# Optimization experiments

Hardware: AMD Instinct MI355X
Metric: run time of the kernel (lower is better)

## Reference

```python
import jax, jax.numpy as jnp
from jax import lax
import numpy as np

INPUT = 80
H1 = 100
H2 = 50


def _lstm_layer(x, Wih, Whh, bih, bhh):
    """PyTorch-semantics single-layer LSTM, batch_first.
    x: [B,T,I]; Wih: [4H,I]; Whh: [4H,H]; biases: [4H]. Gate order: i,f,g,o.
    Returns full hidden sequence [B,T,H]."""
    B, T, _ = x.shape
    H = Whh.shape[1]
    # precompute input projections for all timesteps (one big GEMM)
    pre = jnp.einsum('bti,gi->tbg', x, Wih) + (bih + bhh)  # [T,B,4H]

    def step(carry, p):
        h, c = carry
        gates = p + h @ Whh.T  # [B,4H]
        i, f, g, o = jnp.split(gates, 4, axis=-1)
        i = jax.nn.sigmoid(i)
        f = jax.nn.sigmoid(f)
        g = jnp.tanh(g)
        o = jax.nn.sigmoid(o)
        c = f * c + i * g
        h = o * jnp.tanh(c)
        return (h, c), h

    h0 = jnp.zeros((B, H), x.dtype)
    (_, _), hs = lax.scan(step, (h0, h0), pre)  # hs: [T,B,H]
    return jnp.transpose(hs, (1, 0, 2))  # [B,T,H]


def setup_inputs() -> dict:
    key = jax.random.key(0)
    ks = jax.random.split(key, 9)
    B, T = 1024, 512
    s1 = 1.0 / np.sqrt(H1)
    s2 = 1.0 / np.sqrt(H2)
    return {
        'x': jax.random.normal(ks[0], (B, T, INPUT), dtype=jnp.float32),
        'Wih1': jax.random.uniform(ks[1], (4 * H1, INPUT), jnp.float32, -s1, s1),
        'Whh1': jax.random.uniform(ks[2], (4 * H1, H1), jnp.float32, -s1, s1),
        'bih1': jax.random.uniform(ks[3], (4 * H1,), jnp.float32, -s1, s1),
        'bhh1': jax.random.uniform(ks[4], (4 * H1,), jnp.float32, -s1, s1),
        'Wih2': jax.random.uniform(ks[5], (4 * H2, H1), jnp.float32, -s2, s2),
        'Whh2': jax.random.uniform(ks[6], (4 * H2, H2), jnp.float32, -s2, s2),
        'bih2': jax.random.uniform(ks[7], (4 * H2,), jnp.float32, -s2, s2),
        'bhh2': jax.random.uniform(ks[8], (4 * H2,), jnp.float32, -s2, s2),
    }


def reference(x, Wih1, Whh1, bih1, bhh1, Wih2, Whh2, bih2, bhh2):
    # Dropout layers are identity in eval mode.
    h1 = _lstm_layer(x, Wih1, Whh1, bih1, bhh1)   # [B,T,100]
    h2 = _lstm_layer(h1, Wih2, Whh2, bih2, bhh2)  # [B,T,50]
    return h2[:, -1, :]                            # [B,50]
```

## Files before the change

kernel.cpp:

```cpp
#include <hip/hip_runtime.h>

#define BT 1024
#define TT 512

__device__ __forceinline__ float sig_(float x) { return 1.f / (1.f + __expf(-x)); }
__device__ __forceinline__ float th_(float x)  { return 1.f - 2.f / (1.f + __expf(2.f * x)); }

template <int KS, int KPAD, int KH, int N, bool XMODE>
__device__ __forceinline__ void gp_stage(
    const float* __restrict__ A, const float* __restrict__ W,
    float (&As)[128][KPAD], float (&Bs)[KPAD][128],
    int tid, int n0, int by, int t0, int k0)
{
    constexpr int NQH = KH / 4;
#pragma unroll
    for (int ii = tid; ii < 128 * NQH; ii += 256) {
        int r = ii / NQH, q = ii % NQH;
        const float* src;
        if (XMODE) {
            int b  = (by & 7) * 128 + r;
            int tl = by >> 3;
            src = A + ((size_t)b * TT + (t0 + tl)) * KS;
        } else {
            src = A + (size_t)(by * 128 + r) * KS;
        }
        *(float4*)&As[r][q * 4] = *(const float4*)(src + k0 + q * 4);
    }
#pragma unroll
    for (int ii = tid; ii < 128 * NQH; ii += 256) {
        int n = ii & 127, kq = ii >> 7;
        float4 v = make_float4(0.f, 0.f, 0.f, 0.f);
        if (n0 + n < N) v = *(const float4*)(W + (size_t)(n0 + n) * KS + k0 + kq * 4);
        Bs[kq * 4 + 0][n] = v.x; Bs[kq * 4 + 1][n] = v.y;
        Bs[kq * 4 + 2][n] = v.z; Bs[kq * 4 + 3][n] = v.w;
    }
}

template <int KPAD, int KH>
__device__ __forceinline__ void gp_compute(
    const float (&As)[128][KPAD], const float (&Bs)[KPAD][128],
    float (&acc)[8][8], int tx, int ty)
{
    for (int kk = 0; kk < KH; kk += 4) {
        float4 bv[4][2];
#pragma unroll
        for (int r = 0; r < 4; r++) {
            bv[r][0] = *(const float4*)&Bs[kk + r][tx * 8];
            bv[r][1] = *(const float4*)&Bs[kk + r][tx * 8 + 4];
        }
#pragma unroll
        for (int i = 0; i < 8; i++) {
            float4 av = *(const float4*)&As[ty + 16 * i][kk];
#pragma unroll
            for (int s = 0; s < 2; s++) {
                acc[i][s*4+0] = fmaf(av.x, bv[0][s].x, acc[i][s*4+0]);
                acc[i][s*4+0] = fmaf(av.y, bv[1][s].x, acc[i][s*4+0]);
                acc[i][s*4+0] = fmaf(av.z, bv[2][s].x, acc[i][s*4+0]);
                acc[i][s*4+0] = fmaf(av.w, bv[3][s].x, acc[i][s*4+0]);
                acc[i][s*4+1] = fmaf(av.x, bv[0][s].y, acc[i][s*4+1]);
                acc[i][s*4+1] = fmaf(av.y, bv[1][s].y, acc[i][s*4+1]);
                acc[i][s*4+1] = fmaf(av.z, bv[2][s].y, acc[i][s*4+1]);
                acc[i][s*4+1] = fmaf(av.w, bv[3][s].y, acc[i][s*4+1]);
                acc[i][s*4+2] = fmaf(av.x, bv[0][s].z, acc[i][s*4+2]);
                acc[i][s*4+2] = fmaf(av.y, bv[1][s].z, acc[i][s*4+2]);
                acc[i][s*4+2] = fmaf(av.z, bv[2][s].z, acc[i][s*4+2]);
                acc[i][s*4+2] = fmaf(av.w, bv[3][s].z, acc[i][s*4+2]);
                acc[i][s*4+3] = fmaf(av.x, bv[0][s].w, acc[i][s*4+3]);
                acc[i][s*4+3] = fmaf(av.y, bv[1][s].w, acc[i][s*4+3]);
                acc[i][s*4+3] = fmaf(av.z, bv[2][s].w, acc[i][s*4+3]);
                acc[i][s*4+3] = fmaf(av.w, bv[3][s].w, acc[i][s*4+3]);
            }
        }
    }
}

template <int KS, int KPAD, int KH0, int N, bool XMODE>
__global__ __launch_bounds__(256, 3) void gemm_pre(
    const float* __restrict__ A, const float* __restrict__ W,
    const float* __restrict__ bih, const float* __restrict__ bhh,
    float* __restrict__ out, int t0)
{
    constexpr int KH1 = KS - KH0;
    __shared__ __align__(16) float As[128][KPAD];
    __shared__ __align__(16) float Bs[KPAD][128];
    const int tid = threadIdx.x;
    const int n0 = blockIdx.x * 128;
    const int by = blockIdx.y;
    const int Rbase = by * 128;
    const int tx = tid & 15, ty = tid >> 4;

    float acc[8][8];
#pragma unroll
    for (int i = 0; i < 8; i++)
#pragma unroll
        for (int j = 0; j < 8; j++) acc[i][j] = 0.f;

    gp_stage<KS, KPAD, KH0, N, XMODE>(A, W, As, Bs, tid, n0, by, t0, 0);
    __syncthreads();
    gp_compute<KPAD, KH0>(As, Bs, acc, tx, ty);
    __syncthreads();
    gp_stage<KS, KPAD, KH1, N, XMODE>(A, W, As, Bs, tid, n0, by, t0, KH0);
    __syncthreads();
    gp_compute<KPAD, KH1>(As, Bs, acc, tx, ty);

#pragma unroll
    for (int s = 0; s < 2; s++) {
        int n = n0 + tx * 8 + s * 4;
        if (n < N) {
            float4 bias;
            bias.x = bih[n] + bhh[n];         bias.y = bih[n + 1] + bhh[n + 1];
            bias.z = bih[n + 2] + bhh[n + 2]; bias.w = bih[n + 3] + bhh[n + 3];
#pragma unroll
            for (int i = 0; i < 8; i++) {
                size_t R = (size_t)Rbase + ty + 16 * i;
                float4 o;
                o.x = acc[i][s*4+0] + bias.x; o.y = acc[i][s*4+1] + bias.y;
                o.z = acc[i][s*4+2] + bias.z; o.w = acc[i][s*4+3] + bias.w;
                *(float4*)(out + R * N + n) = o;
            }
        }
    }
}

__global__ __launch_bounds__(512, 4) void rec1(
    const float* __restrict__ pre,
    const float* __restrict__ Whh,
    float* __restrict__ hseq,
    float* __restrict__ cst,
    int Tc, int first)
{
    __shared__ __align__(16) float hs[2][100];
    __shared__ __align__(16) float pres[2][800];
    __shared__ float gbuf[5 * 4 * 2 * 100];
    const int tid = threadIdx.x;
    const int b0 = blockIdx.x * 2;

    const bool comp = tid < 500;
    const int j  = tid % 100;
    const int kq = tid / 100;

    float4 w[4][5];
    if (comp) {
#pragma unroll
        for (int g = 0; g < 4; g++) {
            const float4* W4 = (const float4*)(Whh + (size_t)(g * 100 + j) * 100);
#pragma unroll
            for (int q = 0; q < 5; q++) w[g][q] = W4[kq * 5 + q];
        }
    }

    const bool upd = tid < 200;
    const int ub = tid / 100, uj = tid % 100;
    float c = 0.f;
    if (upd) {
        float h = 0.f;
        if (!first) {
            h = hseq[((size_t)(Tc - 1) * BT + b0 + ub) * 100 + uj];
            c = cst[(size_t)(b0 + ub) * 100 + uj];
        }
        hs[ub][uj] = h;
        ((float4*)pres[0])[tid] = ((const float4*)(pre + (size_t)b0 * 400))[tid];
    }
    __syncthreads();

    int cur = 0;
    for (int t = 0; t < Tc; t++) {
        int tn = (t + 1 < Tc) ? (t + 1) : t;
        float4 pf0;
        if (upd)
            pf0 = ((const float4*)(pre + (size_t)tn * BT * 400 + (size_t)b0 * 400))[tid];

        if (comp) {
            float acc[4][2];
#pragma unroll
            for (int g = 0; g < 4; g++) { acc[g][0] = 0.f; acc[g][1] = 0.f; }
            const float4* h0 = (const float4*)hs[0];
            const float4* h1 = (const float4*)hs[1];
#pragma unroll
            for (int q = 0; q < 5; q++) {
                int f = kq * 5 + q;
                float4 v0 = h0[f], v1 = h1[f];
#pragma unroll
                for (int g = 0; g < 4; g++) {
                    float4 wq = w[g][q];
                    acc[g][0] = fmaf(wq.x, v0.x, acc[g][0]);
                    acc[g][0] = fmaf(wq.y, v0.y, acc[g][0]);
                    acc[g][0] = fmaf(wq.z, v0.z, acc[g][0]);
                    acc[g][0] = fmaf(wq.w, v0.w, acc[g][0]);
                    acc[g][1] = fmaf(wq.x, v1.x, acc[g][1]);
                    acc[g][1] = fmaf(wq.y, v1.y, acc[g][1]);
                    acc[g][1] = fmaf(wq.z, v1.z, acc[g][1]);
                    acc[g][1] = fmaf(wq.w, v1.w, acc[g][1]);
                }
            }
#pragma unroll
            for (int g = 0; g < 4; g++) {
                gbuf[((kq * 4 + g) * 2 + 0) * 100 + j] = acc[g][0];
                gbuf[((kq * 4 + g) * 2 + 1) * 100 + j] = acc[g][1];
            }
        }
        __syncthreads();

        if (upd) {
            const float* pb = pres[cur];
            float s0 = 0.f, s1 = 0.f, s2 = 0.f, s3 = 0.f;
#pragma unroll
            for (int q = 0; q < 5; q++) {
                int base = q * 800;
                s0 += gbuf[base + (0 * 2 + ub) * 100 + uj];
                s1 += gbuf[base + (1 * 2 + ub) * 100 + uj];
                s2 += gbuf[base + (2 * 2 + ub) * 100 + uj];
                s3 += gbuf[base + (3 * 2 + ub) * 100 + uj];
            }
            float xi = s0 + pb[ub * 400 + uj];
            float xf = s1 + pb[ub * 400 + 100 + uj];
            float xg = s2 + pb[ub * 400 + 200 + uj];
            float xo = s3 + pb[ub * 400 + 300 + uj];
            float ii = sig_(xi), ff = sig_(xf), gg = th_(xg), oo = sig_(xo);
            c = ff * c + ii * gg;
            float h = oo * th_(c);
            hs[ub][uj] = h;
            hseq[((size_t)t * BT + b0 + ub) * 100 + uj] = h;
            ((float4*)pres[cur ^ 1])[tid] = pf0;
        }
        __syncthreads();
        cur ^= 1;
    }
    if (upd) cst[(size_t)(b0 + ub) * 100 + uj] = c;
}

__global__ __launch_bounds__(256, 4) void rec2(
    const float* __restrict__ pre2,
    const float* __restrict__ Whh,
    float* __restrict__ cst, float* __restrict__ hst,
    float* __restrict__ out,
    int Tc, int first)
{
    __shared__ __align__(16) float hs[2][50];
    __shared__ __align__(16) float pres[2][400];
    __shared__ float gbuf[5 * 4 * 2 * 50];
    const int tid = threadIdx.x;
    const int b0 = blockIdx.x * 2;

    const bool comp = tid < 250;
    const int j  = tid % 50;
    const int kq = tid / 50;

    float2 w[4][5];
    if (comp) {
#pragma unroll
        for (int g = 0; g < 4; g++) {
            const float2* W2 = (const float2*)(Whh + (size_t)(g * 50 + j) * 50);
#pragma unroll
            for (int q = 0; q < 5; q++) w[g][q] = W2[kq * 5 + q];
        }
    }

    const bool upd = tid < 100;
    const int ub = tid / 50, uj = tid % 50;
    float c = 0.f, hlast = 0.f;
    if (upd) {
        float h = 0.f;
        if (!first) {
            h = hst[(size_t)(b0 + ub) * 50 + uj];
            c = cst[(size_t)(b0 + ub) * 50 + uj];
        }
        hs[ub][uj] = h;
        hlast = h;
        ((float4*)pres[0])[tid] = ((const float4*)(pre2 + (size_t)b0 * 200))[tid];
    }
    __syncthreads();

    int cur = 0;
    for (int t = 0; t < Tc; t++) {
        int tn = (t + 1 < Tc) ? (t + 1) : t;
        float4 pf0;
        if (upd)
            pf0 = ((const float4*)(pre2 + (size_t)tn * BT * 200 + (size_t)b0 * 200))[tid];

        if (comp) {
            float acc[4][2];
#pragma unroll
            for (int g = 0; g < 4; g++) { acc[g][0] = 0.f; acc[g][1] = 0.f; }
            const float2* hA = (const float2*)hs[0];
            const float2* hB = (const float2*)hs[1];
#pragma unroll
            for (int q = 0; q < 5; q++) {
                int f = kq * 5 + q;
                float2 v0 = hA[f], v1 = hB[f];
#pragma unroll
                for (int g = 0; g < 4; g++) {
                    float2 wq = w[g][q];
                    acc[g][0] = fmaf(wq.x, v0.x, acc[g][0]);
                    acc[g][0] = fmaf(wq.y, v0.y, acc[g][0]);
                    acc[g][1] = fmaf(wq.x, v1.x, acc[g][1]);
                    acc[g][1] = fmaf(wq.y, v1.y, acc[g][1]);
                }
            }
#pragma unroll
            for (int g = 0; g < 4; g++) {
                gbuf[((kq * 4 + g) * 2 + 0) * 50 + j] = acc[g][0];
                gbuf[((kq * 4 + g) * 2 + 1) * 50 + j] = acc[g][1];
            }
        }
        __syncthreads();

        if (upd) {
            const float* pb = pres[cur];
            float s0 = 0.f, s1 = 0.f, s2 = 0.f, s3 = 0.f;
#pragma unroll
            for (int q = 0; q < 5; q++) {
                int base = q * 400;
                s0 += gbuf[base + (0 * 2 + ub) * 50 + uj];
                s1 += gbuf[base + (1 * 2 + ub) * 50 + uj];
                s2 += gbuf[base + (2 * 2 + ub) * 50 + uj];
                s3 += gbuf[base + (3 * 2 + ub) * 50 + uj];
            }
            float xi = s0 + pb[ub * 200 + uj];
            float xf = s1 + pb[ub * 200 + 50 + uj];
            float xg = s2 + pb[ub * 200 + 100 + uj];
            float xo = s3 + pb[ub * 200 + 150 + uj];
            float ii = sig_(xi), ff = sig_(xf), gg = th_(xg), oo = sig_(xo);
            c = ff * c + ii * gg;
            float h = oo * th_(c);
            hs[ub][uj] = h;
            hlast = h;
            ((float4*)pres[cur ^ 1])[tid] = pf0;
        }
        __syncthreads();
        cur ^= 1;
    }
    if (upd) {
        cst[(size_t)(b0 + ub) * 50 + uj] = c;
        hst[(size_t)(b0 + ub) * 50 + uj] = hlast;
        out[(size_t)(b0 + ub) * 50 + uj] = hlast;
    }
}

extern "C" void kernel_launch(void* const* d_in, const int* in_sizes, int n_in,
                              void* d_out, int out_size, void* d_ws, size_t ws_size,
                              hipStream_t stream)
{
    const float* x    = (const float*)d_in[0];
    const float* Wih1 = (const float*)d_in[1];
    const float* Whh1 = (const float*)d_in[2];
    const float* bih1 = (const float*)d_in[3];
    const float* bhh1 = (const float*)d_in[4];
    const float* Wih2 = (const float*)d_in[5];
    const float* Whh2 = (const float*)d_in[6];
    const float* bih2 = (const float*)d_in[7];
    const float* bhh2 = (const float*)d_in[8];
    float* out = (float*)d_out;
    float* ws  = (float*)d_ws;

    int Tc = 64;
    auto need = [](int tc) -> size_t {
        return ((size_t)tc * 1024 * (400 + 100 + 200) +
                (size_t)1024 * 100 + (size_t)1024 * 50 * 2) * sizeof(float);
    };
    while (Tc > 1 && need(Tc) > ws_size) Tc >>= 1;

    float* pre1 = ws;
    float* h1s  = pre1 + (size_t)Tc * 1024 * 400;
    float* pre2 = h1s  + (size_t)Tc * 1024 * 100;
    float* c1   = pre2 + (size_t)Tc * 1024 * 200;
    float* c2   = c1 + 1024 * 100;
    float* h2st = c2 + 1024 * 50;

    const int nch = TT / Tc;
    for (int ch = 0; ch < nch; ch++) {
        int t0 = ch * Tc;
        gemm_pre<80, 40, 40, 400, true ><<<dim3(4, Tc * 8), 256, 0, stream>>>(
            x, Wih1, bih1, bhh1, pre1, t0);
        rec1<<<dim3(512), dim3(512), 0, stream>>>(pre1, Whh1, h1s, c1, Tc, ch == 0 ? 1 : 0);
        gemm_pre<100, 52, 52, 200, false><<<dim3(2, Tc * 8), 256, 0, stream>>>(
            h1s, Wih2, bih2, bhh2, pre2, 0);
        rec2<<<dim3(512), dim3(256), 0, stream>>>(pre2, Whh2, c2, h2st, out, Tc, ch == 0 ? 1 : 0);
    }
}
```

Baseline: 2.529 ms.

## Overlap layer-2 recurrence of previous chunk with layer-1 recurrence in fused kernel

Moves the two LSTM recurrence bodies into device functions that share one shared-memory union. A combined kernel runs layer-1 on chunk ch in its first 512 blocks and layer-2 on chunk ch-1 in 256 extra blocks, each handling two 256-thread groups. The launch order becomes a software pipeline: prologue, steady state, epilogue, with the layer-2 input GEMM issued before pre1 is overwritten. The goal is to hide the latency-bound sequential recurrences of both layers behind each other instead of running them back to back. The cost is more complex chunk dependencies and a larger grid competing for CU resources.

```diff
diff --git a/kernel.cpp b/kernel.cpp
--- a/kernel.cpp
+++ b/kernel.cpp
@@ -122,19 +122,23 @@
     }
 }
 
-__global__ __launch_bounds__(512, 4) void rec1(
-    const float* __restrict__ pre,
-    const float* __restrict__ Whh,
-    float* __restrict__ hseq,
-    float* __restrict__ cst,
-    int Tc, int first)
-{
-    __shared__ __align__(16) float hs[2][100];
-    __shared__ __align__(16) float pres[2][800];
-    __shared__ float gbuf[5 * 4 * 2 * 100];
-    const int tid = threadIdx.x;
-    const int b0 = blockIdx.x * 2;
-
+struct __align__(16) R1S {
+    float hs[2][100];
+    float pres[2][800];
+    float gbuf[5 * 4 * 2 * 100];
+};
+struct __align__(16) R2S {
+    float hs[2][50];
+    float pres[2][400];
+    float gbuf[5 * 4 * 2 * 50];
+};
+union __align__(16) FS { R1S r1; R2S r2[2]; };
+
+__device__ __forceinline__ void rec1_body(
+    R1S& s, int tid, int b0,
+    const float* __restrict__ pre, const float* __restrict__ Whh,
+    float* __restrict__ hseq, float* __restrict__ cst, int Tc, int first)
+{
     const bool comp = tid < 500;
     const int j  = tid % 100;
     const int kq = tid / 100;
@@ -158,8 +162,8 @@
             h = hseq[((size_t)(Tc - 1) * BT + b0 + ub) * 100 + uj];
             c = cst[(size_t)(b0 + ub) * 100 + uj];
         }
-        hs[ub][uj] = h;
-        ((float4*)pres[0])[tid] = ((const float4*)(pre + (size_t)b0 * 400))[tid];
+        s.hs[ub][uj] = h;
+        ((float4*)s.pres[0])[tid] = ((const float4*)(pre + (size_t)b0 * 400))[tid];
     }
     __syncthreads();
 
@@ -174,8 +178,8 @@
             float acc[4][2];
 #pragma unroll
             for (int g = 0; g < 4; g++) { acc[g][0] = 0.f; acc[g][1] = 0.f; }
-            const float4* h0 = (const float4*)hs[0];
-            const float4* h1 = (const float4*)hs[1];
+            const float4* h0 = (const float4*)s.hs[0];
+            const float4* h1 = (const float4*)s.hs[1];
 #pragma unroll
             for (int q = 0; q < 5; q++) {
                 int f = kq * 5 + q;
@@ -195,22 +199,22 @@
             }
 #pragma unroll
             for (int g = 0; g < 4; g++) {
-                gbuf[((kq * 4 + g) * 2 + 0) * 100 + j] = acc[g][0];
-                gbuf[((kq * 4 + g) * 2 + 1) * 100 + j] = acc[g][1];
+                s.gbuf[((kq * 4 + g) * 2 + 0) * 100 + j] = acc[g][0];
+                s.gbuf[((kq * 4 + g) * 2 + 1) * 100 + j] = acc[g][1];
             }
         }
         __syncthreads();
 
         if (upd) {
-            const float* pb = pres[cur];
+            const float* pb = s.pres[cur];
             float s0 = 0.f, s1 = 0.f, s2 = 0.f, s3 = 0.f;
 #pragma unroll
             for (int q = 0; q < 5; q++) {
                 int base = q * 800;
-                s0 += gbuf[base + (0 * 2 + ub) * 100 + uj];
-                s1 += gbuf[base + (1 * 2 + ub) * 100 + uj];
-                s2 += gbuf[base + (2 * 2 + ub) * 100 + uj];
-                s3 += gbuf[base + (3 * 2 + ub) * 100 + uj];
+                s0 += s.gbuf[base + (0 * 2 + ub) * 100 + uj];
+                s1 += s.gbuf[base + (1 * 2 + ub) * 100 + uj];
+                s2 += s.gbuf[base + (2 * 2 + ub) * 100 + uj];
+                s3 += s.gbuf[base + (3 * 2 + ub) * 100 + uj];
             }
             float xi = s0 + pb[ub * 400 + uj];
             float xf = s1 + pb[ub * 400 + 100 + uj];
@@ -219,9 +223,9 @@
             float ii = sig_(xi), ff = sig_(xf), gg = th_(xg), oo = sig_(xo);
             c = ff * c + ii * gg;
             float h = oo * th_(c);
-            hs[ub][uj] = h;
+            s.hs[ub][uj] = h;
             hseq[((size_t)t * BT + b0 + ub) * 100 + uj] = h;
-            ((float4*)pres[cur ^ 1])[tid] = pf0;
+            ((float4*)s.pres[cur ^ 1])[tid] = pf0;
         }
         __syncthreads();
         cur ^= 1;
@@ -229,19 +233,12 @@
     if (upd) cst[(size_t)(b0 + ub) * 100 + uj] = c;
 }
 
-__global__ __launch_bounds__(256, 4) void rec2(
-    const float* __restrict__ pre2,
-    const float* __restrict__ Whh,
-    float* __restrict__ cst, float* __restrict__ hst,
-    float* __restrict__ out,
+__device__ __forceinline__ void rec2_body(
+    R2S& s, int tid, int b0,
+    const float* __restrict__ pre2, const float* __restrict__ Whh,
+    float* __restrict__ cst, float* __restrict__ hst, float* __restrict__ out,
     int Tc, int first)
 {
-    __shared__ __align__(16) float hs[2][50];
-    __shared__ __align__(16) float pres[2][400];
-    __shared__ float gbuf[5 * 4 * 2 * 50];
-    const int tid = threadIdx.x;
-    const int b0 = blockIdx.x * 2;
-
     const bool comp = tid < 250;
     const int j  = tid % 50;
     const int kq = tid / 50;
@@ -265,9 +262,9 @@
             h = hst[(size_t)(b0 + ub) * 50 + uj];
             c = cst[(size_t)(b0 + ub) * 50 + uj];
         }
-        hs[ub][uj] = h;
+        s.hs[ub][uj] = h;
         hlast = h;
-        ((float4*)pres[0])[tid] = ((const float4*)(pre2 + (size_t)b0 * 200))[tid];
+        ((float4*)s.pres[0])[tid] = ((const float4*)(pre2 + (size_t)b0 * 200))[tid];
     }
     __syncthreads();
 
@@ -282,8 +279,8 @@
             float acc[4][2];
 #pragma unroll
             for (int g = 0; g < 4; g++) { acc[g][0] = 0.f; acc[g][1] = 0.f; }
-            const float2* hA = (const float2*)hs[0];
-            const float2* hB = (const float2*)hs[1];
+            const float2* hA = (const float2*)s.hs[0];
+            const float2* hB = (const float2*)s.hs[1];
 #pragma unroll
             for (int q = 0; q < 5; q++) {
                 int f = kq * 5 + q;
@@ -299,22 +296,22 @@
             }
 #pragma unroll
             for (int g = 0; g < 4; g++) {
-                gbuf[((kq * 4 + g) * 2 + 0) * 50 + j] = acc[g][0];
-                gbuf[((kq * 4 + g) * 2 + 1) * 50 + j] = acc[g][1];
+                s.gbuf[((kq * 4 + g) * 2 + 0) * 50 + j] = acc[g][0];
+                s.gbuf[((kq * 4 + g) * 2 + 1) * 50 + j] = acc[g][1];
             }
         }
         __syncthreads();
 
         if (upd) {
-            const float* pb = pres[cur];
+            const float* pb = s.pres[cur];
             float s0 = 0.f, s1 = 0.f, s2 = 0.f, s3 = 0.f;
 #pragma unroll
             for (int q = 0; q < 5; q++) {
                 int base = q * 400;
-                s0 += gbuf[base + (0 * 2 + ub) * 50 + uj];
-                s1 += gbuf[base + (1 * 2 + ub) * 50 + uj];
-                s2 += gbuf[base + (2 * 2 + ub) * 50 + uj];
-                s3 += gbuf[base + (3 * 2 + ub) * 50 + uj];
+                s0 += s.gbuf[base + (0 * 2 + ub) * 50 + uj];
+                s1 += s.gbuf[base + (1 * 2 + ub) * 50 + uj];
+                s2 += s.gbuf[base + (2 * 2 + ub) * 50 + uj];
+                s3 += s.gbuf[base + (3 * 2 + ub) * 50 + uj];
             }
             float xi = s0 + pb[ub * 200 + uj];
             float xf = s1 + pb[ub * 200 + 50 + uj];
@@ -323,9 +320,9 @@
             float ii = sig_(xi), ff = sig_(xf), gg = th_(xg), oo = sig_(xo);
             c = ff * c + ii * gg;
             float h = oo * th_(c);
-            hs[ub][uj] = h;
+            s.hs[ub][uj] = h;
             hlast = h;
-            ((float4*)pres[cur ^ 1])[tid] = pf0;
+            ((float4*)s.pres[cur ^ 1])[tid] = pf0;
         }
         __syncthreads();
         cur ^= 1;
@@ -335,6 +332,34 @@
         hst[(size_t)(b0 + ub) * 50 + uj] = hlast;
         out[(size_t)(b0 + ub) * 50 + uj] = hlast;
     }
+}
+
+__global__ __launch_bounds__(512, 4) void rec_fused(
+    const float* __restrict__ pre1, const float* __restrict__ Whh1,
+    float* __restrict__ h1seq, float* __restrict__ c1, int first1,
+    const float* __restrict__ pre2, const float* __restrict__ Whh2,
+    float* __restrict__ c2, float* __restrict__ h2st, float* __restrict__ out,
+    int first2, int Tc)
+{
+    __shared__ FS sm;
+    const int bx = blockIdx.x;
+    const int tid = threadIdx.x;
+    if (bx < 512) {
+        rec1_body(sm.r1, tid, bx * 2, pre1, Whh1, h1seq, c1, Tc, first1);
+    } else {
+        const int h = tid >> 8;
+        rec2_body(sm.r2[h], tid & 255, (bx - 512) * 4 + h * 2,
+                  pre2, Whh2, c2, h2st, out, Tc, first2);
+    }
+}
+
+__global__ __launch_bounds__(256, 4) void rec2k(
+    const float* __restrict__ pre2, const float* __restrict__ Whh,
+    float* __restrict__ cst, float* __restrict__ hst, float* __restrict__ out,
+    int Tc, int first)
+{
+    __shared__ R2S s;
+    rec2_body(s, threadIdx.x, blockIdx.x * 2, pre2, Whh, cst, hst, out, Tc, first);
 }
 
 extern "C" void kernel_launch(void* const* d_in, const int* in_sizes, int n_in,
@@ -368,13 +393,25 @@
     float* h2st = c2 + 1024 * 50;
 
     const int nch = TT / Tc;
-    for (int ch = 0; ch < nch; ch++) {
+
+    gemm_pre<80, 40, 40, 400, true ><<<dim3(4, Tc * 8), 256, 0, stream>>>(
+        x, Wih1, bih1, bhh1, pre1, 0);
+    rec_fused<<<dim3(512), dim3(512), 0, stream>>>(
+        pre1, Whh1, h1s, c1, 1, pre2, Whh2, c2, h2st, out, 0, Tc);
+
+    for (int ch = 1; ch < nch; ch++) {
         int t0 = ch * Tc;
+        gemm_pre<100, 52, 52, 200, false><<<dim3(2, Tc * 8), 256, 0, stream>>>(
+            h1s, Wih2, bih2, bhh2, pre2, 0);
         gemm_pre<80, 40, 40, 400, true ><<<dim3(4, Tc * 8), 256, 0, stream>>>(
             x, Wih1, bih1, bhh1, pre1, t0);
-        rec1<<<dim3(512), dim3(512), 0, stream>>>(pre1, Whh1, h1s, c1, Tc, ch == 0 ? 1 : 0);
-        gemm_pre<100, 52, 52, 200, false><<<dim3(2, Tc * 8), 256, 0, stream>>>(
-            h1s, Wih2, bih2, bhh2, pre2, 0);
-        rec2<<<dim3(512), dim3(256), 0, stream>>>(pre2, Whh2, c2, h2st, out, Tc, ch == 0 ? 1 : 0);
-    }
-}
+        rec_fused<<<dim3(768), dim3(512), 0, stream>>>(
+            pre1, Whh1, h1s, c1, 0,
+            pre2, Whh2, c2, h2st, out, (ch == 1) ? 1 : 0, Tc);
+    }
+
+    gemm_pre<100, 52, 52, 200, false><<<dim3(2, Tc * 8), 256, 0, stream>>>(
+        h1s, Wih2, bih2, bhh2, pre2, 0);
+    rec2k<<<dim3(512), dim3(256), 0, stream>>>(
+        pre2, Whh2, c2, h2st, out, Tc, 0);
+}
```

Measured after the change: 2.458 ms. 2.8% less time.
